# Optimization experiments

Measured on AMD Instinct MI355X. Metric: run time of the kernel, lower is better.

## Reference

```python
import jax, jax.numpy as jnp
import numpy as np

D_IN, H, NH = 256, 512, 8
B, T = 8, 1024


def sinusoidal_pe(seq_len, d_model):
    pos = jnp.arange(seq_len, dtype=jnp.float32)[:, None]
    div = jnp.exp(jnp.arange(0, d_model, 2, dtype=jnp.float32) * (-jnp.log(10000.0) / d_model))
    pe = jnp.zeros((seq_len, d_model), jnp.float32)
    pe = pe.at[:, 0::2].set(jnp.sin(pos * div)).at[:, 1::2].set(jnp.cos(pos * div))
    return pe


def layer_norm(x, g, b, eps=1e-5):
    mu = jnp.mean(x, -1, keepdims=True)
    var = jnp.mean((x - mu) ** 2, -1, keepdims=True)
    return (x - mu) * jax.lax.rsqrt(var + eps) * g + b


def lstm_dir(x, wih, whh, bih, bhh):
    # x: [B,T,H]; wih/whh: [4H,H]; gate order i,f,g,o (PyTorch convention)
    Bx = x.shape[0]
    Hh = whh.shape[1]
    xg = jnp.einsum('bth,gh->btg', x, wih) + bih  # precompute input gates [B,T,4H]

    def step(carry, xg_t):
        h, c = carry
        gates = xg_t + h @ whh.T + bhh
        i, f, g, o = jnp.split(gates, 4, axis=-1)
        c = jax.nn.sigmoid(f) * c + jax.nn.sigmoid(i) * jnp.tanh(g)
        h = jax.nn.sigmoid(o) * jnp.tanh(c)
        return (h, c), h

    h0 = jnp.zeros((Bx, Hh), x.dtype)
    _, hs = jax.lax.scan(step, (h0, h0), xg.transpose(1, 0, 2))
    return hs.transpose(1, 0, 2)  # [B,T,H]


def setup_inputs():
    key = jax.random.key(0)
    ks = jax.random.split(key, 30)
    s = 0.02

    def g(k, shape):
        return jax.random.normal(k, shape, jnp.float32) * s

    return {
        'temporal_data': jax.random.normal(ks[0], (B, T, D_IN), jnp.float32),
        'w_in': g(ks[1], (H, D_IN)), 'b_in': jnp.zeros((H,), jnp.float32),
        'wq': g(ks[2], (H, H)), 'bq': jnp.zeros((H,), jnp.float32),
        'wk': g(ks[3], (H, H)), 'bk': jnp.zeros((H,), jnp.float32),
        'wv': g(ks[4], (H, H)), 'bv': jnp.zeros((H,), jnp.float32),
        'wo': g(ks[5], (H, H)), 'bo': jnp.zeros((H,), jnp.float32),
        'g1': jnp.ones((H,), jnp.float32), 'b1': jnp.zeros((H,), jnp.float32),
        'wih_f': g(ks[6], (4 * H, H)), 'whh_f': g(ks[7], (4 * H, H)),
        'bih_f': jnp.zeros((4 * H,), jnp.float32), 'bhh_f': jnp.zeros((4 * H,), jnp.float32),
        'wih_b': g(ks[8], (4 * H, H)), 'whh_b': g(ks[9], (4 * H, H)),
        'bih_b': jnp.zeros((4 * H,), jnp.float32), 'bhh_b': jnp.zeros((4 * H,), jnp.float32),
        'g2': jnp.ones((2 * H,), jnp.float32), 'b2': jnp.zeros((2 * H,), jnp.float32),
        'w_out': g(ks[10], (H, 2 * H)), 'b_out': jnp.zeros((H,), jnp.float32),
    }


def reference(temporal_data, w_in, b_in, wq, bq, wk, bk, wv, bv, wo, bo, g1, b1,
              wih_f, whh_f, bih_f, bhh_f, wih_b, whh_b, bih_b, bhh_b, g2, b2, w_out, b_out):
    x = temporal_data @ w_in.T + b_in                      # [B,T,H]
    Bx, Tx, _ = x.shape
    x = x + sinusoidal_pe(Tx, H)
    residual = x

    hd = H // NH
    q = (x @ wq.T + bq).reshape(Bx, Tx, NH, hd).transpose(0, 2, 1, 3)
    k = (x @ wk.T + bk).reshape(Bx, Tx, NH, hd).transpose(0, 2, 1, 3)
    v = (x @ wv.T + bv).reshape(Bx, Tx, NH, hd).transpose(0, 2, 1, 3)
    scores = jnp.einsum('bhqd,bhkd->bhqk', q, k) * (hd ** -0.5)
    causal = jnp.triu(jnp.ones((Tx, Tx), bool), 1)
    scores = jnp.where(causal, jnp.float32(-1e9), scores)
    attn = jax.nn.softmax(scores, axis=-1)
    o = jnp.einsum('bhqk,bhkd->bhqd', attn, v).transpose(0, 2, 1, 3).reshape(Bx, Tx, H)
    o = o @ wo.T + bo

    x = layer_norm(o + residual, g1, b1)                   # dropout in eval = identity

    h_fwd = lstm_dir(x, wih_f, whh_f, bih_f, bhh_f)
    h_bwd = jnp.flip(lstm_dir(jnp.flip(x, 1), wih_b, whh_b, bih_b, bhh_b), 1)
    lstm_out = jnp.concatenate([h_fwd, h_bwd], axis=-1)    # [B,T,2H]
    lstm_out = layer_norm(lstm_out, g2, b2)

    emb = jnp.mean(lstm_out, axis=1)                       # [B,2H]
    return emb @ w_out.T + b_out                           # [B,H]
```

## Files before the change

### kernel.cpp

```cpp
#include <hip/hip_runtime.h>

typedef unsigned short u16;
typedef unsigned int   u32;
typedef unsigned long long u64;
typedef __attribute__((ext_vector_type(8))) short short8v;
typedef __attribute__((ext_vector_type(4))) float f32x4;
typedef __attribute__((ext_vector_type(4))) unsigned int u32x4;

#define DINL __device__ __forceinline__

DINL u16 f2bf(float f){ union{float f;u32 u;} v{f}; return (u16)((v.u + 0x7fffu + ((v.u>>16)&1u))>>16); }
DINL float bf2f(u16 b){ union{u32 u;float f;} v{(u32)b<<16}; return v.f; }
DINL f32x4 MFMA16(short8v a, short8v b, f32x4 c){ return __builtin_amdgcn_mfma_f32_16x16x32_bf16(a,b,c,0,0,0); }
DINL void gl16(const void* g, void* l){
  __builtin_amdgcn_global_load_lds((const __attribute__((address_space(1))) void*)g,
                                   (__attribute__((address_space(3))) void*)l, 16, 0, 0);
}
DINL float wredd(float v){
#pragma unroll
  for (int m=1;m<64;m<<=1) v += __shfl_xor(v, m);
  return v;
}
DINL float sigm(float x){ return 1.f/(1.f+__expf(-x)); }
DINL float tanh_(float x){ return 2.f/(1.f+__expf(-2.f*x)) - 1.f; }

__global__ __launch_bounds__(256) void zerok(u32* __restrict__ dst){
  size_t i = ((size_t)blockIdx.x*256 + threadIdx.x)*4;
  u32x4 z = {0,0,0,0};
  *(u32x4*)(dst + i) = z;
}

__global__ __launch_bounds__(256) void cvtk(const float* __restrict__ src, u16* __restrict__ dst, int n){
  int i = (blockIdx.x*256 + threadIdx.x)*4;
  float4 v = *(const float4*)(src + i);
  dst[i+0]=f2bf(v.x); dst[i+1]=f2bf(v.y); dst[i+2]=f2bf(v.z); dst[i+3]=f2bf(v.w);
}

template<int EPI>
__global__ __launch_bounds__(256) void gemm128(
    const u16* __restrict__ A, const u16* __restrict__ W,
    const float* __restrict__ bias0, const float* __restrict__ bias1, const float* __restrict__ bias2,
    const u16* __restrict__ resid, u16* __restrict__ out, int M, int N, int K)
{
  __shared__ __align__(16) u16 Al[128*64];
  __shared__ __align__(16) u16 Bl[128*64];
  const int tid = threadIdx.x, lane = tid & 63, w = tid >> 6;
  const int wr = w >> 1, wc = w & 1;
  const int m0 = blockIdx.y * 128, n0 = blockIdx.x * 128;
  f32x4 acc[4][4] = {};
  for (int k0 = 0; k0 < K; k0 += 64) {
#pragma unroll
    for (int j = 0; j < 4; ++j) {
      int idx = (j*4 + w)*64 + lane;
      int r = idx >> 3, c8 = idx & 7;
      gl16(A + (size_t)(m0 + r)*K + k0 + c8*8, (void*)(Al + (size_t)(j*4+w)*512));
      gl16(W + (size_t)(n0 + r)*K + k0 + c8*8, (void*)(Bl + (size_t)(j*4+w)*512));
    }
    __syncthreads();
#pragma unroll
    for (int kk = 0; kk < 2; ++kk) {
      short8v af[4], bf[4];
#pragma unroll
      for (int i = 0; i < 4; ++i)
        af[i] = *(const short8v*)(Al + ((wr*64 + i*16 + (lane&15))*64 + kk*32 + (lane>>4)*8));
#pragma unroll
      for (int i = 0; i < 4; ++i)
        bf[i] = *(const short8v*)(Bl + ((wc*64 + i*16 + (lane&15))*64 + kk*32 + (lane>>4)*8));
#pragma unroll
      for (int mi=0;mi<4;++mi)
#pragma unroll
        for (int ni=0;ni<4;++ni)
          acc[mi][ni] = MFMA16(af[mi], bf[ni], acc[mi][ni]);
    }
    __syncthreads();
  }
#pragma unroll
  for (int mi=0;mi<4;++mi)
#pragma unroll
    for (int ni=0;ni<4;++ni)
#pragma unroll
      for (int r=0;r<4;++r) {
        int m = m0 + wr*64 + mi*16 + (lane>>4)*4 + r;
        int n = n0 + wc*64 + ni*16 + (lane&15);
        float v = acc[mi][ni][r];
        if constexpr (EPI == 0) {
          int t = m & 1023;
          float ang = (float)t * expf((float)(n & ~1) * (-9.210340371976184f/512.f));
          v += bias0[n] + ((n & 1) ? cosf(ang) : sinf(ang));
          out[(size_t)m*512 + n] = f2bf(v);
        } else if constexpr (EPI == 1) {
          int g = n >> 9, n5 = n & 511, hh = n5 >> 6, dh = n5 & 63;
          v += (g==0 ? bias0 : g==1 ? bias1 : bias2)[n5];
          size_t bh = (size_t)((m>>10)*8 + hh);
          u16 val = f2bf(v);
          if (g == 0)      out[(bh*1024 + (m&1023))*64 + dh] = val;
          else if (g == 1) out[4194304 + (bh*1024 + (m&1023))*64 + dh] = val;
          else             out[8388608 + (bh*64 + dh)*1024 + (m&1023)] = val;
        } else {
          v += bias0[n] + bf2f(resid[(size_t)m*512 + n]);
          out[(size_t)m*512 + n] = f2bf(v);
        }
      }
}

__global__ __launch_bounds__(256) void attnk(const u16* __restrict__ qb, const u16* __restrict__ kb,
                                             const u16* __restrict__ vt, u16* __restrict__ attno)
{
  __shared__ __align__(16) u16 P[4][16][72];
  const int tid = threadIdx.x, lane = tid & 63, w = tid >> 6;
  const int bh = blockIdx.x >> 4, qblk = blockIdx.x & 15;
  const int b = bh >> 3, h = bh & 7;
  const float scale = 0.125f;
  short8v qf[2];
  {
    const u16* qbase = qb + ((size_t)bh*1024 + qblk*64 + w*16)*64;
#pragma unroll
    for (int kk=0;kk<2;++kk)
      qf[kk] = *(const short8v*)(qbase + (size_t)(lane&15)*64 + kk*32 + (lane>>4)*8);
  }
  f32x4 o[4] = {};
  float mrun[4], lrun[4];
#pragma unroll
  for (int r=0;r<4;++r){ mrun[r] = -1e30f; lrun[r] = 0.f; }
  for (int kblk = 0; kblk <= qblk; ++kblk) {
    f32x4 s[4] = {};
#pragma unroll
    for (int kk=0;kk<2;++kk)
#pragma unroll
      for (int nt=0;nt<4;++nt) {
        short8v kf = *(const short8v*)(kb + ((size_t)bh*1024 + kblk*64 + nt*16 + (lane&15))*64 + kk*32 + (lane>>4)*8);
        s[nt] = MFMA16(qf[kk], kf, s[nt]);
      }
    float pnew[4][4];
#pragma unroll
    for (int r=0;r<4;++r) {
      int q = qblk*64 + w*16 + (lane>>4)*4 + r;
      float sv[4]; float rowmax = -1e30f;
#pragma unroll
      for (int nt=0;nt<4;++nt) {
        int key = kblk*64 + nt*16 + (lane&15);
        float x = s[nt][r]*scale;
        if (key > q) x = -1e30f;
        sv[nt] = x; rowmax = fmaxf(rowmax, x);
      }
#pragma unroll
      for (int msk=1; msk<16; msk<<=1) rowmax = fmaxf(rowmax, __shfl_xor(rowmax, msk));
      float mnew = fmaxf(mrun[r], rowmax);
      float sf = __expf(mrun[r]-mnew);
      float psum = 0.f;
#pragma unroll
      for (int nt=0;nt<4;++nt){ float p = __expf(sv[nt]-mnew); pnew[nt][r]=p; psum += p; }
#pragma unroll
      for (int msk=1; msk<16; msk<<=1) psum += __shfl_xor(psum, msk);
      lrun[r] = lrun[r]*sf + psum;
      mrun[r] = mnew;
#pragma unroll
      for (int nt=0;nt<4;++nt) o[nt][r] *= sf;
    }
#pragma unroll
    for (int nt=0;nt<4;++nt)
#pragma unroll
      for (int r=0;r<4;++r)
        P[w][(lane>>4)*4+r][nt*16+(lane&15)] = f2bf(pnew[nt][r]);
#pragma unroll
    for (int kk=0;kk<2;++kk) {
      short8v pf = *(const short8v*)&P[w][lane&15][kk*32 + (lane>>4)*8];
#pragma unroll
      for (int nt=0;nt<4;++nt) {
        short8v vf = *(const short8v*)(vt + ((size_t)bh*64 + nt*16 + (lane&15))*1024 + kblk*64 + kk*32 + (lane>>4)*8);
        o[nt] = MFMA16(pf, vf, o[nt]);
      }
    }
  }
#pragma unroll
  for (int nt=0;nt<4;++nt)
#pragma unroll
    for (int r=0;r<4;++r) {
      int q = qblk*64 + w*16 + (lane>>4)*4 + r;
      int dh = nt*16 + (lane&15);
      attno[((size_t)b*1024 + q)*512 + h*64 + dh] = f2bf(o[nt][r] / lrun[r]);
    }
}

__global__ __launch_bounds__(256) void ln1k(const u16* __restrict__ pre, const float* __restrict__ g1,
                                            const float* __restrict__ b1, u16* __restrict__ xl){
  int row = blockIdx.x*4 + (threadIdx.x>>6), lane = threadIdx.x&63;
  short8v xv = *(const short8v*)(pre + (size_t)row*512 + lane*8);
  float v[8], s=0.f, s2=0.f;
#pragma unroll
  for (int e=0;e<8;++e){ v[e]=bf2f((u16)xv[e]); s+=v[e]; s2+=v[e]*v[e]; }
  s = wredd(s); s2 = wredd(s2);
  float mu = s*(1.f/512.f);
  float rs = rsqrtf(s2*(1.f/512.f) - mu*mu + 1e-5f);
  int b = row>>10, t = row&1023;
  short8v ov;
#pragma unroll
  for (int e=0;e<8;++e){ int c=lane*8+e; ov[e]=(short)f2bf((v[e]-mu)*rs*g1[c]+b1[c]); }
  *(short8v*)(xl + ((size_t)t*8 + b)*512 + lane*8) = ov;
}

__global__ __launch_bounds__(256) void lstmk(
    const u16* __restrict__ xl,
    const float* __restrict__ wih_f, const float* __restrict__ whh_f,
    const float* __restrict__ bih_f, const float* __restrict__ bhh_f,
    const float* __restrict__ wih_b, const float* __restrict__ whh_b,
    const float* __restrict__ bih_b, const float* __restrict__ bhh_b,
    u32* __restrict__ hx, u16* __restrict__ hs)
{
  extern __shared__ char smem[];
  u16*  WI  = (u16*)smem;
  u16*  WH  = (u16*)(smem + 65536);
  float* RED = (float*)(smem + 131072);

  const int tid = threadIdx.x, lane = tid&63, w = tid>>6;
  const int d = blockIdx.x >> 5, slice = blockIdx.x & 31, u0 = slice*16;
  const float* WIHg = d ? wih_b : wih_f;
  const float* WHHg = d ? whh_b : whh_f;
  const float* BIH  = d ? bih_b : bih_f;
  const float* BHH  = d ? bhh_b : bhh_f;

  for (int f = tid; f < 4096; f += 256) {
    int nt = f>>10, kc = (f>>6)&15, l = f&63;
    size_t grow = (size_t)(nt*512 + u0 + (l&15));
    int k = kc*32 + (l>>4)*8;
    const float* pi = WIHg + grow*512 + k;
    const float* ph = WHHg + grow*512 + k;
    short8v wa, wb;
#pragma unroll
    for (int e=0;e<8;++e){ wa[e]=(short)f2bf(pi[e]); wb[e]=(short)f2bf(ph[e]); }
    *(short8v*)(WI + (size_t)f*8) = wa;
    *(short8v*)(WH + (size_t)f*8) = wb;
  }
  __syncthreads();

  const bool act = tid < 128;
  const int b_ = tid>>4, u_ = tid&15;
  float c_state = 0.f, bias_c[4];
  if (act)
#pragma unroll
    for (int g=0;g<4;++g) bias_c[g] = BIH[g*512+u0+u_] + BHH[g*512+u0+u_];

  for (int t = 0; t < 1024; ++t) {
    const int te = d ? 1023 - t : t;
    f32x4 acc[4] = {};
    {
      const u16* xb = xl + ((size_t)te*8 + (lane&7))*512;
#pragma unroll
      for (int kk=0;kk<4;++kk) {
        const int kc = w*4 + kk;
        short8v xf = *(const short8v*)(xb + kc*32 + (lane>>4)*8);
#pragma unroll
        for (int nt=0;nt<4;++nt)
          acc[nt] = MFMA16(xf, *(const short8v*)(WI + ((size_t)(nt*16+kc)*64 + lane)*8), acc[nt]);
      }
    }
    if (t > 0) {
      const u32 tg = (u32)t;
      const u32* pb = hx + ((size_t)d*2 + ((t-1)&1))*4096 + (size_t)(lane&7)*512 + (size_t)w*128 + (lane>>4)*8;
      u32x4 q0,q1,q2,q3,q4,q5,q6,q7;
      for (;;) {
        asm volatile(
          "global_load_dwordx4 %0, %8, off sc0 sc1\n\t"
          "global_load_dwordx4 %1, %8, off offset:16 sc0 sc1\n\t"
          "global_load_dwordx4 %2, %8, off offset:128 sc0 sc1\n\t"
          "global_load_dwordx4 %3, %8, off offset:144 sc0 sc1\n\t"
          "global_load_dwordx4 %4, %8, off offset:256 sc0 sc1\n\t"
          "global_load_dwordx4 %5, %8, off offset:272 sc0 sc1\n\t"
          "global_load_dwordx4 %6, %8, off offset:384 sc0 sc1\n\t"
          "global_load_dwordx4 %7, %8, off offset:400 sc0 sc1\n\t"
          "s_waitcnt vmcnt(0)"
          : "=&v"(q0),"=&v"(q1),"=&v"(q2),"=&v"(q3),
            "=&v"(q4),"=&v"(q5),"=&v"(q6),"=&v"(q7)
          : "v"(pb));
        bool ok = true;
#pragma unroll
        for (int e=0;e<4;++e) {
          ok = ok && ((q0[e]&0xffffu)==tg) && ((q1[e]&0xffffu)==tg)
                  && ((q2[e]&0xffffu)==tg) && ((q3[e]&0xffffu)==tg)
                  && ((q4[e]&0xffffu)==tg) && ((q5[e]&0xffffu)==tg)
                  && ((q6[e]&0xffffu)==tg) && ((q7[e]&0xffffu)==tg);
        }
        if (__all(ok)) break;
        __builtin_amdgcn_s_sleep(1);
      }
      const u32x4 qa[8] = {q0,q1,q2,q3,q4,q5,q6,q7};
#pragma unroll
      for (int kk=0;kk<4;++kk) {
        short8v hf;
#pragma unroll
        for (int e=0;e<4;++e) {
          hf[e]   = (short)(qa[2*kk][e]   >> 16);
          hf[4+e] = (short)(qa[2*kk+1][e] >> 16);
        }
        const int kc = w*4 + kk;
#pragma unroll
        for (int nt=0;nt<4;++nt)
          acc[nt] = MFMA16(hf, *(const short8v*)(WH + ((size_t)(nt*16+kc)*64 + lane)*8), acc[nt]);
      }
    }
    float* R = RED + (size_t)(t & 1)*2048;
    if (lane < 32)
#pragma unroll
      for (int nt=0;nt<4;++nt)
        *(f32x4*)(R + ((size_t)(w*4+nt)*32 + lane)*4) = acc[nt];
    __syncthreads();
    if (act) {
      const int lc = u_ + 16*(b_>>2), rg = b_&3;
      float gates[4];
#pragma unroll
      for (int g=0;g<4;++g) {
        float s = 0.f;
#pragma unroll
        for (int wv=0;wv<4;++wv) s += R[((size_t)(wv*4+g)*32 + lc)*4 + rg];
        gates[g] = s + bias_c[g];
      }
      float ig = sigm(gates[0]), fg = sigm(gates[1]), gg = tanh_(gates[2]), og = sigm(gates[3]);
      c_state = fg*c_state + ig*gg;
      u16 hv = f2bf(og * tanh_(c_state));
      hs[((size_t)(d*1024 + te)*8 + b_)*512 + u0 + u_] = hv;
      u32 word = ((u32)hv << 16) | (u32)(t + 1);
      u32* dst = hx + ((size_t)d*2 + (t&1))*4096 + (size_t)b_*512 + u0 + u_;
      asm volatile("global_store_dword %0, %1, off sc0 sc1" :: "v"(dst), "v"(word) : "memory");
    }
  }
}

__global__ __launch_bounds__(256) void ln2k(const u16* __restrict__ hs, const float* __restrict__ g2,
                                            const float* __restrict__ b2, float* __restrict__ emb){
  __shared__ float accl[4][1024];
  int b = blockIdx.x>>4, chunk = blockIdx.x&15;
  int lane = threadIdx.x&63, w = threadIdx.x>>6;
  for (int i=lane;i<1024;i+=64) accl[w][i]=0.f;
#pragma unroll 1
  for (int i=0;i<16;++i) {
    int t = chunk*64 + w*16 + i;
    short8v xf = *(const short8v*)(hs + ((size_t)t*8 + b)*512 + lane*8);
    short8v xb = *(const short8v*)(hs + ((size_t)(1024+t)*8 + b)*512 + lane*8);
    float vf[8], vb[8], s=0.f, s2=0.f;
#pragma unroll
    for (int e=0;e<8;++e){ vf[e]=bf2f((u16)xf[e]); vb[e]=bf2f((u16)xb[e]);
                           s += vf[e]+vb[e]; s2 += vf[e]*vf[e]+vb[e]*vb[e]; }
    s = wredd(s); s2 = wredd(s2);
    float mu = s*(1.f/1024.f);
    float rs = rsqrtf(s2*(1.f/1024.f) - mu*mu + 1e-5f);
#pragma unroll
    for (int e=0;e<8;++e){
      int c = lane*8+e;
      accl[w][c]     += (vf[e]-mu)*rs*g2[c]     + b2[c];
      accl[w][512+c] += (vb[e]-mu)*rs*g2[512+c] + b2[512+c];
    }
  }
  __syncthreads();
  for (int c = threadIdx.x; c < 1024; c += 256)
    atomicAdd(emb + (size_t)b*1024 + c, accl[0][c]+accl[1][c]+accl[2][c]+accl[3][c]);
}

__global__ __launch_bounds__(256) void fink(const float* __restrict__ emb, const float* __restrict__ w_out,
                                            const float* __restrict__ b_out, float* __restrict__ out){
  int gid = blockIdx.x*256 + threadIdx.x;
  int n = gid>>3, b = gid&7;
  const float* e = emb + (size_t)b*1024;
  const float* wr = w_out + (size_t)n*1024;
  float s = 0.f;
  for (int k=0;k<1024;k+=4) {
    float4 ev = *(const float4*)(e+k);
    float4 wv = *(const float4*)(wr+k);
    s += ev.x*wv.x + ev.y*wv.y + ev.z*wv.z + ev.w*wv.w;
  }
  out[(size_t)b*512 + n] = b_out[n] + s*(1.f/1024.f);
}

#define OFF_EMB   0u
#define OFF_HX    32768u
#define OFF_A0    98304u
#define OFF_WIN   4292608u
#define OFF_WQKV  4554752u
#define OFF_WO    6127616u
#define OFF_X0B   6651904u
#define OFF_QB    15040512u
#define OFF_PRE   15040512u
#define OFF_XL    23429120u
#define OFF_ATT   40206336u
#define OFF_HS    48594944u

extern "C" void kernel_launch(void* const* d_in, const int* in_sizes, int n_in,
                              void* d_out, int out_size, void* d_ws, size_t ws_size,
                              hipStream_t stream) {
  const float* temporal = (const float*)d_in[0];
  const float* w_in = (const float*)d_in[1];  const float* b_in = (const float*)d_in[2];
  const float* wq = (const float*)d_in[3];    const float* bq = (const float*)d_in[4];
  const float* wk = (const float*)d_in[5];    const float* bk = (const float*)d_in[6];
  const float* wv = (const float*)d_in[7];    const float* bv = (const float*)d_in[8];
  const float* wo = (const float*)d_in[9];    const float* bo = (const float*)d_in[10];
  const float* g1 = (const float*)d_in[11];   const float* b1 = (const float*)d_in[12];
  const float* wih_f = (const float*)d_in[13]; const float* whh_f = (const float*)d_in[14];
  const float* bih_f = (const float*)d_in[15]; const float* bhh_f = (const float*)d_in[16];
  const float* wih_b = (const float*)d_in[17]; const float* whh_b = (const float*)d_in[18];
  const float* bih_b = (const float*)d_in[19]; const float* bhh_b = (const float*)d_in[20];
  const float* g2 = (const float*)d_in[21];   const float* b2 = (const float*)d_in[22];
  const float* w_out = (const float*)d_in[23]; const float* b_out = (const float*)d_in[24];

  char* ws = (char*)d_ws;
  float* EMB = (float*)(ws + OFF_EMB);
  u32* HX   = (u32*)(ws + OFF_HX);
  u16* A0   = (u16*)(ws + OFF_A0);
  u16* WIN  = (u16*)(ws + OFF_WIN);
  u16* WQKV = (u16*)(ws + OFF_WQKV);
  u16* WOb  = (u16*)(ws + OFF_WO);
  u16* X0B  = (u16*)(ws + OFF_X0B);
  u16* QB   = (u16*)(ws + OFF_QB);
  u16* PRE  = (u16*)(ws + OFF_PRE);
  u16* XL   = (u16*)(ws + OFF_XL);
  u16* ATT  = (u16*)(ws + OFF_ATT);
  u16* HS   = (u16*)(ws + OFF_HS);

  (void)hipFuncSetAttribute((const void*)lstmk, hipFuncAttributeMaxDynamicSharedMemorySize, 147456);

  zerok<<<24,256,0,stream>>>((u32*)(ws + OFF_EMB));

  cvtk<<<2048,256,0,stream>>>(temporal, A0, 2097152);
  cvtk<<<128, 256,0,stream>>>(w_in, WIN, 131072);
  cvtk<<<256, 256,0,stream>>>(wq, WQKV,           262144);
  cvtk<<<256, 256,0,stream>>>(wk, WQKV + 262144,  262144);
  cvtk<<<256, 256,0,stream>>>(wv, WQKV + 524288,  262144);
  cvtk<<<256, 256,0,stream>>>(wo, WOb, 262144);

  gemm128<0><<<dim3(4,64), 256, 0, stream>>>(A0, WIN, b_in, nullptr, nullptr, nullptr, X0B, 8192, 512, 256);
  gemm128<1><<<dim3(12,64),256, 0, stream>>>(X0B, WQKV, bq, bk, bv, nullptr, QB, 8192, 1536, 512);
  attnk<<<1024,256,0,stream>>>(QB, QB + 4194304, QB + 8388608, ATT);
  gemm128<3><<<dim3(4,64), 256, 0, stream>>>(ATT, WOb, bo, nullptr, nullptr, X0B, PRE, 8192, 512, 512);
  ln1k<<<2048,256,0,stream>>>(PRE, g1, b1, XL);
  lstmk<<<64,256,147456,stream>>>(XL, wih_f, whh_f, bih_f, bhh_f, wih_b, whh_b, bih_b, bhh_b, HX, HS);
  ln2k<<<128,256,0,stream>>>(HS, g2, b2, EMB);
  fink<<<16,256,0,stream>>>(EMB, w_out, b_out, (float*)d_out);
}
```

Before: 3.578 ms.

## Keep LSTM weights in registers and halve block count for recurrence

The LSTM recurrence kernel now runs 32 blocks of 512 threads, each covering 32 hidden units, down from 64 blocks of 256 threads covering 16 each. Input and recurrent weight fragments are held in VGPRs instead of being staged in LDS, so the per-step MFMA operands no longer need LDS reads. Having fewer blocks means fewer participants in the cross-block spin-wait sync on the hidden state each step. In exchange, the per-block reduction over 8 waves grows, and register pressure is high (32 short8v weight fragments per thread) with a risk of spills.

```diff
diff --git a/kernel.cpp b/kernel.cpp
--- a/kernel.cpp
+++ b/kernel.cpp
@@ -199,7 +199,7 @@
   *(short8v*)(xl + ((size_t)t*8 + b)*512 + lane*8) = ov;
 }
 
-__global__ __launch_bounds__(256) void lstmk(
+__global__ __launch_bounds__(512, 2) void lstmk(
     const u16* __restrict__ xl,
     const float* __restrict__ wih_f, const float* __restrict__ whh_f,
     const float* __restrict__ bih_f, const float* __restrict__ bhh_f,
@@ -207,111 +207,108 @@
     const float* __restrict__ bih_b, const float* __restrict__ bhh_b,
     u32* __restrict__ hx, u16* __restrict__ hs)
 {
-  extern __shared__ char smem[];
-  u16*  WI  = (u16*)smem;
-  u16*  WH  = (u16*)(smem + 65536);
-  float* RED = (float*)(smem + 131072);
+  extern __shared__ float RED[];
 
   const int tid = threadIdx.x, lane = tid&63, w = tid>>6;
-  const int d = blockIdx.x >> 5, slice = blockIdx.x & 31, u0 = slice*16;
+  const int d = blockIdx.x >> 4, slice = blockIdx.x & 15, u0 = slice*32;
   const float* WIHg = d ? wih_b : wih_f;
   const float* WHHg = d ? whh_b : whh_f;
   const float* BIH  = d ? bih_b : bih_f;
   const float* BHH  = d ? bhh_b : bhh_f;
 
-  for (int f = tid; f < 4096; f += 256) {
-    int nt = f>>10, kc = (f>>6)&15, l = f&63;
-    size_t grow = (size_t)(nt*512 + u0 + (l&15));
-    int k = kc*32 + (l>>4)*8;
-    const float* pi = WIHg + grow*512 + k;
-    const float* ph = WHHg + grow*512 + k;
-    short8v wa, wb;
-#pragma unroll
-    for (int e=0;e<8;++e){ wa[e]=(short)f2bf(pi[e]); wb[e]=(short)f2bf(ph[e]); }
-    *(short8v*)(WI + (size_t)f*8) = wa;
-    *(short8v*)(WH + (size_t)f*8) = wb;
-  }
-  __syncthreads();
-
-  const bool act = tid < 128;
-  const int b_ = tid>>4, u_ = tid&15;
+  const int l15 = lane&15, l16 = lane>>4;
+
+  short8v wi[8][2], wh[8][2];
+#pragma unroll
+  for (int nt=0; nt<8; ++nt) {
+    const int g = nt>>1, uh = nt&1;
+    const size_t row = (size_t)(g*512 + u0 + uh*16 + l15);
+#pragma unroll
+    for (int kk=0; kk<2; ++kk) {
+      const int k = w*64 + kk*32 + l16*8;
+      const float* pi = WIHg + row*512 + k;
+      const float* ph = WHHg + row*512 + k;
+      float4 a0 = *(const float4*)pi, a1 = *(const float4*)(pi+4);
+      float4 b0 = *(const float4*)ph, b1 = *(const float4*)(ph+4);
+      short8v si, sh;
+      si[0]=(short)f2bf(a0.x); si[1]=(short)f2bf(a0.y); si[2]=(short)f2bf(a0.z); si[3]=(short)f2bf(a0.w);
+      si[4]=(short)f2bf(a1.x); si[5]=(short)f2bf(a1.y); si[6]=(short)f2bf(a1.z); si[7]=(short)f2bf(a1.w);
+      sh[0]=(short)f2bf(b0.x); sh[1]=(short)f2bf(b0.y); sh[2]=(short)f2bf(b0.z); sh[3]=(short)f2bf(b0.w);
+      sh[4]=(short)f2bf(b1.x); sh[5]=(short)f2bf(b1.y); sh[6]=(short)f2bf(b1.z); sh[7]=(short)f2bf(b1.w);
+      wi[nt][kk] = si; wh[nt][kk] = sh;
+    }
+  }
+
+  const bool act = tid < 256;
+  const int b_ = tid>>5, u_ = tid&31;
   float c_state = 0.f, bias_c[4];
   if (act)
 #pragma unroll
     for (int g=0;g<4;++g) bias_c[g] = BIH[g*512+u0+u_] + BHH[g*512+u0+u_];
 
+  __syncthreads();
+
   for (int t = 0; t < 1024; ++t) {
     const int te = d ? 1023 - t : t;
-    f32x4 acc[4] = {};
+    f32x4 acc[8] = {};
     {
-      const u16* xb = xl + ((size_t)te*8 + (lane&7))*512;
-#pragma unroll
-      for (int kk=0;kk<4;++kk) {
-        const int kc = w*4 + kk;
-        short8v xf = *(const short8v*)(xb + kc*32 + (lane>>4)*8);
-#pragma unroll
-        for (int nt=0;nt<4;++nt)
-          acc[nt] = MFMA16(xf, *(const short8v*)(WI + ((size_t)(nt*16+kc)*64 + lane)*8), acc[nt]);
-      }
+      const u16* xb = xl + ((size_t)te*8 + (lane&7))*512 + w*64 + l16*8;
+      short8v xf0 = *(const short8v*)(xb);
+      short8v xf1 = *(const short8v*)(xb + 32);
+#pragma unroll
+      for (int nt=0; nt<8; ++nt) acc[nt] = MFMA16(xf0, wi[nt][0], acc[nt]);
+#pragma unroll
+      for (int nt=0; nt<8; ++nt) acc[nt] = MFMA16(xf1, wi[nt][1], acc[nt]);
     }
     if (t > 0) {
       const u32 tg = (u32)t;
-      const u32* pb = hx + ((size_t)d*2 + ((t-1)&1))*4096 + (size_t)(lane&7)*512 + (size_t)w*128 + (lane>>4)*8;
-      u32x4 q0,q1,q2,q3,q4,q5,q6,q7;
+      const u32* pb = hx + ((size_t)d*2 + ((t-1)&1))*4096 + (size_t)(lane&7)*512 + w*64 + l16*8;
+      u32x4 q0,q1,q2,q3;
       for (;;) {
         asm volatile(
-          "global_load_dwordx4 %0, %8, off sc0 sc1\n\t"
-          "global_load_dwordx4 %1, %8, off offset:16 sc0 sc1\n\t"
-          "global_load_dwordx4 %2, %8, off offset:128 sc0 sc1\n\t"
-          "global_load_dwordx4 %3, %8, off offset:144 sc0 sc1\n\t"
-          "global_load_dwordx4 %4, %8, off offset:256 sc0 sc1\n\t"
-          "global_load_dwordx4 %5, %8, off offset:272 sc0 sc1\n\t"
-          "global_load_dwordx4 %6, %8, off offset:384 sc0 sc1\n\t"
-          "global_load_dwordx4 %7, %8, off offset:400 sc0 sc1\n\t"
+          "global_load_dwordx4 %0, %4, off sc0 sc1\n\t"
+          "global_load_dwordx4 %1, %4, off offset:16 sc0 sc1\n\t"
+          "global_load_dwordx4 %2, %4, off offset:128 sc0 sc1\n\t"
+          "global_load_dwordx4 %3, %4, off offset:144 sc0 sc1\n\t"
           "s_waitcnt vmcnt(0)"
-          : "=&v"(q0),"=&v"(q1),"=&v"(q2),"=&v"(q3),
-            "=&v"(q4),"=&v"(q5),"=&v"(q6),"=&v"(q7)
+          : "=&v"(q0),"=&v"(q1),"=&v"(q2),"=&v"(q3)
           : "v"(pb));
         bool ok = true;
 #pragma unroll
         for (int e=0;e<4;++e) {
           ok = ok && ((q0[e]&0xffffu)==tg) && ((q1[e]&0xffffu)==tg)
-                  && ((q2[e]&0xffffu)==tg) && ((q3[e]&0xffffu)==tg)
-                  && ((q4[e]&0xffffu)==tg) && ((q5[e]&0xffffu)==tg)
-                  && ((q6[e]&0xffffu)==tg) && ((q7[e]&0xffffu)==tg);
+                  && ((q2[e]&0xffffu)==tg) && ((q3[e]&0xffffu)==tg);
         }
         if (__all(ok)) break;
         __builtin_amdgcn_s_sleep(1);
       }
-      const u32x4 qa[8] = {q0,q1,q2,q3,q4,q5,q6,q7};
-#pragma unroll
-      for (int kk=0;kk<4;++kk) {
-        short8v hf;
-#pragma unroll
-        for (int e=0;e<4;++e) {
-          hf[e]   = (short)(qa[2*kk][e]   >> 16);
-          hf[4+e] = (short)(qa[2*kk+1][e] >> 16);
-        }
-        const int kc = w*4 + kk;
-#pragma unroll
-        for (int nt=0;nt<4;++nt)
-          acc[nt] = MFMA16(hf, *(const short8v*)(WH + ((size_t)(nt*16+kc)*64 + lane)*8), acc[nt]);
-      }
-    }
-    float* R = RED + (size_t)(t & 1)*2048;
+      short8v hf0, hf1;
+#pragma unroll
+      for (int e=0;e<4;++e) {
+        hf0[e]   = (short)(q0[e] >> 16);
+        hf0[4+e] = (short)(q1[e] >> 16);
+        hf1[e]   = (short)(q2[e] >> 16);
+        hf1[4+e] = (short)(q3[e] >> 16);
+      }
+#pragma unroll
+      for (int nt=0; nt<8; ++nt) acc[nt] = MFMA16(hf0, wh[nt][0], acc[nt]);
+#pragma unroll
+      for (int nt=0; nt<8; ++nt) acc[nt] = MFMA16(hf1, wh[nt][1], acc[nt]);
+    }
+    float* R = RED + (size_t)(t & 1)*8192;
     if (lane < 32)
 #pragma unroll
-      for (int nt=0;nt<4;++nt)
-        *(f32x4*)(R + ((size_t)(w*4+nt)*32 + lane)*4) = acc[nt];
+      for (int nt=0; nt<8; ++nt)
+        *(f32x4*)(R + ((size_t)(w*8+nt)*32 + lane)*4) = acc[nt];
     __syncthreads();
     if (act) {
-      const int lc = u_ + 16*(b_>>2), rg = b_&3;
+      const int lc = (u_&15) + 16*(b_>>2), rg = b_&3, uh = u_>>4;
       float gates[4];
 #pragma unroll
       for (int g=0;g<4;++g) {
         float s = 0.f;
 #pragma unroll
-        for (int wv=0;wv<4;++wv) s += R[((size_t)(wv*4+g)*32 + lc)*4 + rg];
+        for (int wv=0; wv<8; ++wv) s += R[((size_t)(wv*8 + g*2 + uh)*32 + lc)*4 + rg];
         gates[g] = s + bias_c[g];
       }
       float ig = sigm(gates[0]), fg = sigm(gates[1]), gg = tanh_(gates[2]), og = sigm(gates[3]);
@@ -414,7 +411,7 @@
   u16* ATT  = (u16*)(ws + OFF_ATT);
   u16* HS   = (u16*)(ws + OFF_HS);
 
-  (void)hipFuncSetAttribute((const void*)lstmk, hipFuncAttributeMaxDynamicSharedMemorySize, 147456);
+  (void)hipFuncSetAttribute((const void*)lstmk, hipFuncAttributeMaxDynamicSharedMemorySize, 65536);
 
   zerok<<<24,256,0,stream>>>((u32*)(ws + OFF_EMB));
 
@@ -430,7 +427,7 @@
   attnk<<<1024,256,0,stream>>>(QB, QB + 4194304, QB + 8388608, ATT);
   gemm128<3><<<dim3(4,64), 256, 0, stream>>>(ATT, WOb, bo, nullptr, nullptr, X0B, PRE, 8192, 512, 512);
   ln1k<<<2048,256,0,stream>>>(PRE, g1, b1, XL);
-  lstmk<<<64,256,147456,stream>>>(XL, wih_f, whh_f, bih_f, bhh_f, wih_b, whh_b, bih_b, bhh_b, HX, HS);
+  lstmk<<<32,512,65536,stream>>>(XL, wih_f, whh_f, bih_f, bhh_f, wih_b, whh_b, bih_b, bhh_b, HX, HS);
   ln2k<<<128,256,0,stream>>>(HS, g2, b2, EMB);
   fink<<<16,256,0,stream>>>(EMB, w_out, b_out, (float*)d_out);
 }
```

Measured after the change: 3.399 ms. 5.0% less time.
